# Performance work log

Measured on AMD Instinct MI355X. Metric: run time of the kernel, lower is better.

Reference implementation:

```python
import jax, jax.numpy as jnp
import numpy as np

B, S, H = 2, 2048, 4096
NH, NKV, HD = 32, 8, 128
EPS = 1e-6


def _rope_tables(seq_len, head_dim, base=10000.0):
    inv = 1.0 / (base ** (np.arange(0, head_dim, 2, dtype=np.float32) / head_dim))
    t = np.arange(seq_len, dtype=np.float32)
    freqs = np.outer(t, inv)                       # [S, HD/2]
    emb = np.concatenate([freqs, freqs], axis=-1)  # [S, HD] (HF rotate_half layout)
    return jnp.asarray(np.cos(emb)), jnp.asarray(np.sin(emb))


def setup_inputs() -> dict:
    key = jax.random.key(0)
    ks = jax.random.split(key, 6)
    x = jax.random.normal(ks[0], (B, S, H), dtype=jnp.float32)
    wq = jax.random.normal(ks[1], (NH * HD, H), dtype=jnp.float32) * 0.02
    wk = jax.random.normal(ks[2], (NKV * HD, H), dtype=jnp.float32) * 0.02
    wv = jax.random.normal(ks[3], (NKV * HD, H), dtype=jnp.float32) * 0.02
    wo = jax.random.normal(ks[4], (H, NH * HD), dtype=jnp.float32) * 0.02
    cos1, sin1 = _rope_tables(S, HD)
    cos = jnp.broadcast_to(cos1[None], (B, S, HD))
    sin = jnp.broadcast_to(sin1[None], (B, S, HD))
    return {
        "x": x, "cos": cos, "sin": sin,
        "wq": wq, "wk": wk, "wv": wv, "wo": wo,
        "q_norm_w": jnp.ones((HD,), jnp.float32),
        "k_norm_w": jnp.ones((HD,), jnp.float32),
    }


def _rms_norm(x, w):
    # fp32 RMSNorm over last dim, scaled by per-head-dim weight
    xf = x.astype(jnp.float32)
    n = xf * jax.lax.rsqrt(jnp.mean(xf * xf, axis=-1, keepdims=True) + EPS)
    return n.astype(x.dtype) * w


def _rotate_half(x):
    x1, x2 = jnp.split(x, 2, axis=-1)
    return jnp.concatenate([-x2, x1], axis=-1)


def reference(x, cos, sin, wq, wk, wv, wo, q_norm_w, k_norm_w):
    bs, seqlen, _ = x.shape
    # projections (nn.Linear: y = x @ W^T)
    xq = (x @ wq.T).reshape(bs, seqlen, NH, HD)
    xk = (x @ wk.T).reshape(bs, seqlen, NKV, HD)
    xv = (x @ wv.T).reshape(bs, seqlen, NKV, HD)
    # per-head RMSNorm before RoPE
    xq = _rms_norm(xq, q_norm_w)
    xk = _rms_norm(xk, k_norm_w)
    # [b, h, s, d]
    xq = xq.transpose(0, 2, 1, 3)
    xk = xk.transpose(0, 2, 1, 3)
    xv = xv.transpose(0, 2, 1, 3)
    # RoPE, cos/sin broadcast over heads
    c = cos[:, None, :, :]
    s = sin[:, None, :, :]
    xq = xq * c + _rotate_half(xq) * s
    xk = xk * c + _rotate_half(xk) * s
    # GQA: repeat kv heads
    rep = NH // NKV
    if rep > 1:
        xk = jnp.repeat(xk, rep, axis=1)
        xv = jnp.repeat(xv, rep, axis=1)
    # causal SDPA
    scale = 1.0 / jnp.sqrt(jnp.float32(HD))
    scores = jnp.einsum("bhqd,bhkd->bhqk", xq, xk) * scale
    mask = jnp.tril(jnp.ones((seqlen, seqlen), bool))
    scores = jnp.where(mask, scores, jnp.finfo(scores.dtype).min)
    probs = jax.nn.softmax(scores, axis=-1)
    out = jnp.einsum("bhqk,bhkd->bhqd", probs, xv)
    out = out.transpose(0, 2, 1, 3).reshape(bs, seqlen, NH * HD)
    return out @ wo.T
```

## Files before the change

kernel.cpp:

```cpp
#include <hip/hip_runtime.h>
#include <hip/hip_bf16.h>

#define NB  2
#define SS  2048
#define HH  4096
#define NH  32
#define NKV 8
#define HD  128
#define MR  (NB*SS)

typedef __bf16 bf16x8 __attribute__((ext_vector_type(8)));
typedef float  f32x4  __attribute__((ext_vector_type(4)));
typedef float  f32x16 __attribute__((ext_vector_type(16)));
using bf16 = __hip_bfloat16;

__device__ __forceinline__ f32x4 mfma16(bf16x8 a, bf16x8 b, f32x4 c) {
  return __builtin_amdgcn_mfma_f32_16x16x32_bf16(a, b, c, 0, 0, 0);
}
__device__ __forceinline__ f32x16 mfma32(bf16x8 a, bf16x8 b, f32x16 c) {
  return __builtin_amdgcn_mfma_f32_32x32x16_bf16(a, b, c, 0, 0, 0);
}
__device__ __forceinline__ unsigned cvtpk(float lo, float hi) {
  unsigned r; asm("v_cvt_pk_bf16_f32 %0, %1, %2" : "=v"(r) : "v"(lo), "v"(hi));
  return r;
}
__device__ __forceinline__ void swap32(unsigned &a, unsigned &b) {
  asm volatile("v_permlane32_swap_b32 %0, %1" : "+v"(a), "+v"(b));
}
__device__ __forceinline__ float fexp2(float x) {
  float r; asm("v_exp_f32 %0, %1" : "=v"(r) : "v"(x)); return r;
}

typedef const __attribute__((address_space(1))) void gv_t;
typedef __attribute__((address_space(3))) void lv_t;
__device__ __forceinline__ void gload16(const void* g, void* l) {
  __builtin_amdgcn_global_load_lds((gv_t*)g, (lv_t*)l, 16, 0, 0);
}
#define CFENCE asm volatile("" ::: "memory")

__global__ void f2b5(const float* __restrict__ s0, const float* __restrict__ s1,
                     const float* __restrict__ s2, const float* __restrict__ s3,
                     const float* __restrict__ s4,
                     bf16* __restrict__ d0, bf16* __restrict__ d1,
                     bf16* __restrict__ d2, bf16* __restrict__ d3,
                     bf16* __restrict__ d4)
{
  const unsigned c0 = 4194304u, c1 = 8388608u, c2 = 9437184u, c3 = 10485760u,
                 c4 = 14680064u;
  unsigned i = blockIdx.x*blockDim.x + threadIdx.x;
  unsigned stride = gridDim.x*blockDim.x;
  for (unsigned u = i; u < c4; u += stride) {
    const float* s; bf16* d; unsigned off;
    if (u < c0)      { s = s0; d = d0; off = u; }
    else if (u < c1) { s = s1; d = d1; off = u - c0; }
    else if (u < c2) { s = s2; d = d2; off = u - c1; }
    else if (u < c3) { s = s3; d = d3; off = u - c2; }
    else             { s = s4; d = d4; off = u - c3; }
    float4 v = *(const float4*)(s + (size_t)off*4);
    __hip_bfloat16 b0 = __float2bfloat16(v.x);
    __hip_bfloat16 b1 = __float2bfloat16(v.y);
    __hip_bfloat16 b2 = __float2bfloat16(v.z);
    __hip_bfloat16 b3 = __float2bfloat16(v.w);
    ushort4 o;
    o.x = *reinterpret_cast<unsigned short*>(&b0);
    o.y = *reinterpret_cast<unsigned short*>(&b1);
    o.z = *reinterpret_cast<unsigned short*>(&b2);
    o.w = *reinterpret_cast<unsigned short*>(&b3);
    *(ushort4*)((unsigned short*)d + (size_t)off*4) = o;
  }
}

template<typename OutT>
__global__ __launch_bounds__(512, 2) void gemm256(
    const bf16* __restrict__ A, const bf16* __restrict__ Bt, OutT* __restrict__ C,
    int M, int N, int K, int tilesX)
{
  __shared__ bf16 lds[2*2*2*8192];

  const int bid = blockIdx.x;
  const int cpx = gridDim.x >> 3;
  const int wg  = (bid & 7)*cpx + (bid >> 3);
  const int m0 = (wg / tilesX) * 256, n0 = (wg % tilesX) * 256;

  const int tid = threadIdx.x;
  const int l = tid & 63;
  const int l15 = l & 15, lhi = l >> 4;
  const int wid = tid >> 6;
  const int wr = wid >> 2, wc = wid & 3;

  const int srow = tid >> 2;
  const int sps  = tid & 3;
  const int sls  = (sps - (srow >> 1)) & 3;
  const bf16* ga0 = A  + (size_t)(m0 + srow)*K       + sls*8;
  const bf16* ga1 = A  + (size_t)(m0 + srow + 128)*K + sls*8;
  const bf16* gb0 = Bt + (size_t)(n0 + srow)*K       + sls*8;
  const bf16* gb1 = Bt + (size_t)(n0 + srow + 128)*K + sls*8;
  const int ldst = tid*8;

#define REG(buf, mat, ks) (&lds[(((buf)*2 + (mat))*2 + (ks))*8192])
#define STG_A(buf, ks, kofs) do {                                 \
    gload16(ga0 + (kofs), REG(buf,0,ks) + ldst);                  \
    gload16(ga1 + (kofs), REG(buf,0,ks) + ldst + 4096);           \
  } while (0)
#define STG_B(buf, ks, kofs) do {                                 \
    gload16(gb0 + (kofs), REG(buf,1,ks) + ldst);                  \
    gload16(gb1 + (kofs), REG(buf,1,ks) + ldst + 4096);           \
  } while (0)

  f32x4 acc[8][4];
  #pragma unroll
  for (int fm = 0; fm < 8; ++fm)
    #pragma unroll
    for (int fn = 0; fn < 4; ++fn)
      #pragma unroll
      for (int e = 0; e < 4; ++e) acc[fm][fn][e] = 0.f;

  const int arow = wr*128 + l15;
  const int brow = wc*64  + l15;
  const int psl  = (lhi + (l15 >> 1)) & 3;

#define PHASE(PB, KS, STG, WN) do {                                        \
    const bf16* Ar_ = REG(PB, 0, KS);                                      \
    const bf16* Br_ = REG(PB, 1, KS);                                      \
    bf16x8 af[8], bv[4];                                                   \
    for (int fm = 0; fm < 8; ++fm)                                         \
      af[fm] = *(const bf16x8*)(Ar_ + (arow + fm*16)*32 + psl*8);          \
    for (int fn = 0; fn < 4; ++fn)                                         \
      bv[fn] = *(const bf16x8*)(Br_ + (brow + fn*16)*32 + psl*8);          \
    STG;                                                                   \
    CFENCE;                                                                \
    __builtin_amdgcn_s_barrier();                                          \
    __builtin_amdgcn_s_setprio(1);                                         \
    for (int fm = 0; fm < 8; ++fm)                                         \
      for (int fn = 0; fn < 4; ++fn)                                       \
        acc[fm][fn] = mfma16(af[fm], bv[fn], acc[fm][fn]);                 \
    __builtin_amdgcn_s_setprio(0);                                         \
    if ((WN) == 8)      asm volatile("s_waitcnt vmcnt(8)" ::: "memory");   \
    else if ((WN) == 4) asm volatile("s_waitcnt vmcnt(4)" ::: "memory");   \
    else if ((WN) == 0) asm volatile("s_waitcnt vmcnt(0)" ::: "memory");   \
    __builtin_amdgcn_s_barrier();                                          \
    CFENCE;                                                                \
  } while (0)

  const int nt = K >> 6;

  STG_A(0, 0, 0);  STG_B(0, 0, 0);
  STG_A(0, 1, 32); STG_B(0, 1, 32);
  STG_A(1, 0, 64); STG_B(1, 0, 64);
  asm volatile("s_waitcnt vmcnt(8)" ::: "memory");
  __builtin_amdgcn_s_barrier();
  CFENCE;

  for (int i = 0; i < (nt >> 1) - 1; ++i) {
    const int t  = i << 1;
    const int k1 = ((t + 1) << 6) + 32;
    const int k2 = (t + 2) << 6;
    const int k3 = (t + 3) << 6;
    PHASE(0, 0, { STG_A(1, 1, k1);      STG_B(1, 1, k1);      }, 8);
    PHASE(0, 1, { STG_A(0, 0, k2);      STG_B(0, 0, k2);      }, 8);
    PHASE(1, 0, { STG_A(0, 1, k2 + 32); STG_B(0, 1, k2 + 32); }, 8);
    PHASE(1, 1, { STG_A(1, 0, k3);      STG_B(1, 0, k3);      }, 8);
  }
  {
    const int k1 = ((nt - 1) << 6) + 32;
    PHASE(0, 0, { STG_A(1, 1, k1); STG_B(1, 1, k1); }, 8);
    PHASE(0, 1, (void)0,  4);
    PHASE(1, 0, (void)0,  0);
    PHASE(1, 1, (void)0, -1);
  }
#undef PHASE
#undef STG_A
#undef STG_B
#undef REG

  #pragma unroll
  for (int fm = 0; fm < 8; ++fm) {
    const int crow = m0 + wr*128 + fm*16 + lhi*4;
    #pragma unroll
    for (int fn = 0; fn < 4; ++fn) {
      const int ccol = n0 + wc*64 + fn*16 + l15;
      #pragma unroll
      for (int j = 0; j < 4; ++j) {
        if constexpr (sizeof(OutT) == 2)
          C[(size_t)(crow + j)*N + ccol] = __float2bfloat16(acc[fm][fn][j]);
        else
          C[(size_t)(crow + j)*N + ccol] = acc[fm][fn][j];
      }
    }
  }
}

__global__ __launch_bounds__(512, 2) void gemm128n(
    const bf16* __restrict__ A, const bf16* __restrict__ Bt, bf16* __restrict__ C,
    int M, int N, int K, int tilesX)
{
  __shared__ bf16 lds[2*2*12288];

  const int bid = blockIdx.x;
  const int cpx = gridDim.x >> 3;
  const int wg  = (bid & 7)*cpx + (bid >> 3);
  const int m0 = (wg / tilesX) * 128, n0 = (wg % tilesX) * 256;

  const int tid = threadIdx.x;
  const int l = tid & 63;
  const int l15 = l & 15, lhi = l >> 4;
  const int wid = tid >> 6;
  const int wr = wid >> 2, wc = wid & 3;

  const int srow = tid >> 2;
  const int sps  = tid & 3;
  const int sls  = (sps - (srow >> 1)) & 3;
  const bf16* gaA = A  + (size_t)(m0 + srow)*K       + sls*8;
  const bf16* gb0 = Bt + (size_t)(n0 + srow)*K       + sls*8;
  const bf16* gb1 = Bt + (size_t)(n0 + srow + 128)*K + sls*8;
  const int ldst = tid*8;

#define REGA(buf, ks) (&lds[((buf)*2 + (ks))*12288])
#define REGB(buf, ks) (&lds[((buf)*2 + (ks))*12288 + 4096])
#define STGKA(buf, ks, kofs) gload16(gaA + (kofs), REGA(buf,ks) + ldst)
#define STGKB(buf, ks, kofs) do {                                 \
    gload16(gb0 + (kofs), REGB(buf,ks) + ldst);                   \
    gload16(gb1 + (kofs), REGB(buf,ks) + ldst + 4096);            \
  } while (0)

  f32x4 acc[4][4];
  #pragma unroll
  for (int fm = 0; fm < 4; ++fm)
    #pragma unroll
    for (int fn = 0; fn < 4; ++fn)
      #pragma unroll
      for (int e = 0; e < 4; ++e) acc[fm][fn][e] = 0.f;

  const int arow = wr*64 + l15;
  const int brow = wc*64 + l15;
  const int psl  = (lhi + (l15 >> 1)) & 3;

#define PHASEK(PB, KS, STG, WN) do {                                       \
    const bf16* Ar_ = REGA(PB, KS);                                        \
    const bf16* Br_ = REGB(PB, KS);                                        \
    bf16x8 af[4], bv[4];                                                   \
    for (int fm = 0; fm < 4; ++fm)                                         \
      af[fm] = *(const bf16x8*)(Ar_ + (arow + fm*16)*32 + psl*8);          \
    for (int fn = 0; fn < 4; ++fn)                                         \
      bv[fn] = *(const bf16x8*)(Br_ + (brow + fn*16)*32 + psl*8);          \
    STG;                                                                   \
    CFENCE;                                                                \
    __builtin_amdgcn_s_barrier();                                          \
    __builtin_amdgcn_s_setprio(1);                                         \
    for (int fm = 0; fm < 4; ++fm)                                         \
      for (int fn = 0; fn < 4; ++fn)                                       \
        acc[fm][fn] = mfma16(af[fm], bv[fn], acc[fm][fn]);                 \
    __builtin_amdgcn_s_setprio(0);                                         \
    if ((WN) == 6)      asm volatile("s_waitcnt vmcnt(6)" ::: "memory");   \
    else if ((WN) == 0) asm volatile("s_waitcnt vmcnt(0)" ::: "memory");   \
    __builtin_amdgcn_s_barrier();                                          \
    CFENCE;                                                                \
  } while (0)

  const int nt = K >> 6;

  STGKB(0, 0, 0);  STGKA(0, 0, 0);  STGKB(0, 1, 32);  STGKA(0, 1, 32);
  STGKB(1, 0, 64); STGKA(1, 0, 64); STGKB(1, 1, 96);  STGKA(1, 1, 96);
  asm volatile("s_waitcnt vmcnt(6)" ::: "memory");
  __builtin_amdgcn_s_barrier();
  CFENCE;

  for (int i = 0; i < (nt >> 1) - 1; ++i) {
    const int t  = i << 1;
    const int k2 = (t + 2) << 6;
    const int k3 = (t + 3) << 6;
    PHASEK(0, 0, { STGKB(0, 0, k2);      STGKA(0, 0, k2);      }, -1);
    PHASEK(0, 1, { STGKB(0, 1, k2 + 32); STGKA(0, 1, k2 + 32); },  6);
    PHASEK(1, 0, { STGKB(1, 0, k3);      STGKA(1, 0, k3);      }, -1);
    PHASEK(1, 1, { STGKB(1, 1, k3 + 32); STGKA(1, 1, k3 + 32); },  6);
  }
  {
    PHASEK(0, 0, (void)0, -1);
    PHASEK(0, 1, (void)0,  0);
    PHASEK(1, 0, (void)0, -1);
    PHASEK(1, 1, (void)0, -1);
  }
#undef PHASEK
#undef STGKA
#undef STGKB
#undef REGA
#undef REGB

  #pragma unroll
  for (int fm = 0; fm < 4; ++fm) {
    const int crow = m0 + wr*64 + fm*16 + lhi*4;
    #pragma unroll
    for (int fn = 0; fn < 4; ++fn) {
      const int ccol = n0 + wc*64 + fn*16 + l15;
      #pragma unroll
      for (int j = 0; j < 4; ++j)
        C[(size_t)(crow + j)*N + ccol] = __float2bfloat16(acc[fm][fn][j]);
    }
  }
}

__global__ __launch_bounds__(256) void normrope(
    const bf16* __restrict__ src, bf16* __restrict__ dst,
    const float* __restrict__ cosb, const float* __restrict__ sinb,
    const float* __restrict__ w, int nh, float scale, int rowstride, int coloff)
{
  const int wid = threadIdx.x >> 6, lane = threadIdx.x & 63;
  const int row = blockIdx.x*4 + wid;
  const int m = row / nh, h = row % nh;
  const int b = m / SS, s = m % SS;
  const bf16* sp = src + (size_t)m*rowstride + coloff + h*HD;
  float v1 = __bfloat162float(sp[lane]);
  float v2 = __bfloat162float(sp[lane + 64]);
  float ss = v1*v1 + v2*v2;
  #pragma unroll
  for (int msk = 1; msk < 64; msk <<= 1) ss += __shfl_xor(ss, msk);
  float r = rsqrtf(ss*(1.f/128.f) + 1e-6f) * scale;
  float n1 = v1*r*w[lane], n2 = v2*r*w[lane + 64];
  const float* cp  = cosb + (size_t)m*HD;
  const float* sip = sinb + (size_t)m*HD;
  float o1 = n1*cp[lane]      - n2*sip[lane];
  float o2 = n2*cp[lane + 64] + n1*sip[lane + 64];
  bf16* dp = dst + ((size_t)(b*nh + h)*SS + s)*HD;
  dp[lane]      = __float2bfloat16(o1);
  dp[lane + 64] = __float2bfloat16(o2);
}

__global__ __launch_bounds__(256) void vtrans(const bf16* __restrict__ v0,
                                              bf16* __restrict__ vt,
                                              int rowstride, int coloff)
{
  __shared__ bf16 tile[64][65];
  const int s0 = blockIdx.x*64, d0 = blockIdx.y*64, bkv = blockIdx.z;
  const int bb = bkv >> 3, kv = bkv & 7;
  const int c = threadIdx.x & 63, rbase = threadIdx.x >> 6;
  #pragma unroll
  for (int r = 0; r < 64; r += 4) {
    int sl = r + rbase;
    tile[sl][c] = v0[(size_t)(bb*SS + s0 + sl)*rowstride + coloff + kv*HD + d0 + c];
  }
  __syncthreads();
  #pragma unroll
  for (int r = 0; r < 64; r += 4) {
    int dl = r + rbase;
    vt[((size_t)bkv*HD + d0 + dl)*SS + s0 + c] = tile[c][dl];
  }
}

__global__ __launch_bounds__(512, 2) void attn_fwd(
    const bf16* __restrict__ qr, const bf16* __restrict__ kr,
    const bf16* __restrict__ vt, bf16* __restrict__ ao)
{
  __shared__ __align__(16) char smem[65536];

  const int L = blockIdx.x;
  const int orig = (L & 7)*64 + (L >> 3);
  const int bh = orig >> 3, j = orig & 7;
  const int b = bh >> 5, h = bh & 31, kvh = h >> 2;

  const int tid = threadIdx.x;
  const int wid = tid >> 6, lane = tid & 63;
  const int l31 = lane & 31, hi = lane >> 5;
  const unsigned hi16 = hi << 4;
  const unsigned swz = (lane & 7) << 4;

  const int qw0 = (wid < 4) ? (j*128 + wid*32) : ((15 - j)*128 + (wid - 4)*32);
  const int NT = 32 - 2*j;
  const int qlane = qw0 + l31;

  const bf16* Qp = qr + ((size_t)(b*NH + h)*SS + qlane)*HD;
  const bf16* Kp = kr + (size_t)(b*NKV + kvh)*SS*HD;
  const bf16* Vp = vt + (size_t)(b*NKV + kvh)*HD*SS;

  const int krA = tid >> 4;
  const int ksA = tid & 15;
  const int vrA = tid >> 3;
  const int vsA = tid & 7;
  const int kswz = (ksA ^ (krA & 7))*8;
  const int vswz = (vsA ^ (vrA & 7))*8;

#define STAGE_ATTN(buf, kvbase) do {                                        \
    char* kb = smem + (buf)*32768;                                          \
    char* vb = kb + 16384;                                                  \
    gload16(Kp + (size_t)(krA + (kvbase))*HD + kswz,      kb + tid*16);     \
    gload16(Kp + (size_t)(krA + 32 + (kvbase))*HD + kswz, kb + 8192 + tid*16); \
    gload16(Vp + (size_t)vrA*SS + (kvbase) + vswz,        vb + tid*16);     \
    gload16(Vp + (size_t)(vrA + 64)*SS + (kvbase) + vswz, vb + 8192 + tid*16); \
  } while (0)

  STAGE_ATTN(0, 0);
  bf16x8 qf[8];
  #pragma unroll
  for (int kd = 0; kd < 8; ++kd)
    qf[kd] = *(const bf16x8*)(Qp + kd*16 + hi*8);
  asm volatile("s_waitcnt vmcnt(0)" ::: "memory");
  __builtin_amdgcn_s_barrier();
  CFENCE;

  f32x16 o0, o1, o2, o3;
  #pragma unroll
  for (int r = 0; r < 16; ++r) { o0[r] = 0.f; o1[r] = 0.f; o2[r] = 0.f; o3[r] = 0.f; }
  float mrow = -1e30f, lrow = 0.f;

  for (int t = 0; t < NT; ++t) {
    const int p = t & 1;
    const char* KsB = smem + p*32768;
    const char* VsB = KsB + 16384;
    if (t + 1 < NT) STAGE_ATTN(p ^ 1, (t + 1)*64);
    const int kv0 = t*64;

    if (kv0 <= qw0 + 31) {
      f32x16 s0, s1;
      #pragma unroll
      for (int r = 0; r < 16; ++r) { s0[r] = 0.f; s1[r] = 0.f; }
      __builtin_amdgcn_s_setprio(1);
      #pragma unroll
      for (int kd = 0; kd < 8; ++kd) {
        bf16x8 k0f = *(const bf16x8*)(KsB + l31*256        + (((unsigned)(kd*32) + hi16) ^ swz));
        bf16x8 k1f = *(const bf16x8*)(KsB + (32 + l31)*256 + (((unsigned)(kd*32) + hi16) ^ swz));
        s0 = mfma32(k0f, qf[kd], s0);
        s1 = mfma32(k1f, qf[kd], s1);
      }
      __builtin_amdgcn_s_setprio(0);
      if (kv0 + 63 > qw0) {
        #pragma unroll
        for (int r = 0; r < 16; ++r) {
          const int off = (r & 3) + 8*(r >> 2) + 4*hi;
          if (kv0 + off > qlane)      s0[r] = -1e30f;
          if (kv0 + 32 + off > qlane) s1[r] = -1e30f;
        }
      }
      float mg[8];
      #pragma unroll
      for (int r = 0; r < 8; ++r)
        mg[r] = fmaxf(fmaxf(s0[r], s0[r + 8]), fmaxf(s1[r], s1[r + 8]));
      float ta = fmaxf(fmaxf(mg[0], mg[1]), mg[2]);
      float tb = fmaxf(fmaxf(mg[3], mg[4]), mg[5]);
      float tmax = fmaxf(fmaxf(ta, tb), fmaxf(mg[6], mg[7]));
      tmax = fmaxf(tmax, __shfl_xor(tmax, 32));
      if (!__all(tmax <= mrow + 8.f)) {
        float mnew = fmaxf(mrow, tmax);
        float alpha = fexp2(mrow - mnew);
        mrow = mnew;
        lrow *= alpha;
        #pragma unroll
        for (int r = 0; r < 16; ++r) {
          o0[r] *= alpha; o1[r] *= alpha; o2[r] *= alpha; o3[r] *= alpha;
        }
      }
      float tsum = 0.f;
      #pragma unroll
      for (int r = 0; r < 16; ++r) { s0[r] = fexp2(s0[r] - mrow); tsum += s0[r]; }
      #pragma unroll
      for (int r = 0; r < 16; ++r) { s1[r] = fexp2(s1[r] - mrow); tsum += s1[r]; }
      tsum += __shfl_xor(tsum, 32);
      lrow += tsum;

      #pragma unroll
      for (int ks = 0; ks < 4; ++ks) {
        const int bb0 = (ks & 1)*8;
        float p0,p1,p2,p3,p4,p5,p6,p7;
        if (ks < 2) { p0=s0[bb0+0];p1=s0[bb0+1];p2=s0[bb0+2];p3=s0[bb0+3];
                      p4=s0[bb0+4];p5=s0[bb0+5];p6=s0[bb0+6];p7=s0[bb0+7]; }
        else        { p0=s1[bb0+0];p1=s1[bb0+1];p2=s1[bb0+2];p3=s1[bb0+3];
                      p4=s1[bb0+4];p5=s1[bb0+5];p6=s1[bb0+6];p7=s1[bb0+7]; }
        unsigned c01 = cvtpk(p0,p1), c23 = cvtpk(p2,p3);
        unsigned c45 = cvtpk(p4,p5), c67 = cvtpk(p6,p7);
        unsigned w0 = c01, w2 = c45; swap32(w0, w2);
        unsigned w1 = c23, w3 = c67; swap32(w1, w3);
        union { unsigned u[4]; bf16x8 v; } pa;
        pa.u[0]=w0; pa.u[1]=w1; pa.u[2]=w2; pa.u[3]=w3;
        __builtin_amdgcn_s_setprio(1);
        #pragma unroll
        for (int dt = 0; dt < 4; ++dt) {
          bf16x8 vf = *(const bf16x8*)(VsB + (dt*32 + l31)*128 +
                                       (((unsigned)(ks*32) + hi16) ^ swz));
          f32x16 &oo = (dt==0)?o0:(dt==1)?o1:(dt==2)?o2:o3;
          oo = mfma32(vf, pa.v, oo);
        }
        __builtin_amdgcn_s_setprio(0);
      }
    }

    asm volatile("s_waitcnt vmcnt(0)" ::: "memory");
    __builtin_amdgcn_s_barrier();
    CFENCE;
  }
#undef STAGE_ATTN

  const float invl = 1.f / lrow;
  char* ow = smem + wid*4096;
  bf16* aop = ao + ((size_t)b*SS + qlane)*HH + h*HD;
  const unsigned eswz = (l31 & 7) << 4;
  #pragma unroll
  for (int half = 0; half < 2; ++half) {
    #pragma unroll
    for (int hh = 0; hh < 2; ++hh) {
      #pragma unroll
      for (int r = 0; r < 16; ++r) {
        const int dcol = hh*32 + (r & 3) + 8*(r >> 2) + 4*hi;
        float val = ((half*2+hh)==0 ? o0[r] : (half*2+hh)==1 ? o1[r]
                     : (half*2+hh)==2 ? o2[r] : o3[r]) * invl;
        *(bf16*)(ow + l31*128 + (((unsigned)(dcol*2)) ^ eswz)) = __float2bfloat16(val);
      }
    }
    #pragma unroll
    for (int m = 0; m < 4; ++m) {
      const int c0 = hi*32 + m*8;
      bf16x8 vv = *(const bf16x8*)(ow + l31*128 + (((unsigned)(c0*2)) ^ eswz));
      *(bf16x8*)(aop + half*64 + c0) = vv;
    }
  }
}

extern "C" void kernel_launch(void* const* d_in, const int* in_sizes, int n_in,
                              void* d_out, int out_size, void* d_ws, size_t ws_size,
                              hipStream_t stream)
{
  const float* x    = (const float*)d_in[0];
  const float* cosb = (const float*)d_in[1];
  const float* sinb = (const float*)d_in[2];
  const float* wq   = (const float*)d_in[3];
  const float* wk   = (const float*)d_in[4];
  const float* wv   = (const float*)d_in[5];
  const float* wo   = (const float*)d_in[6];
  const float* qnw  = (const float*)d_in[7];
  const float* knw  = (const float*)d_in[8];
  float* out = (float*)d_out;

  char* ws = (char*)d_ws;
  bf16* xb    = (bf16*)(ws);
  bf16* wqkvb = (bf16*)(ws +  33554432);
  bf16* wob   = (bf16*)(ws +  83886080);
  bf16* q0    = (bf16*)(ws + 117440512);
  bf16* kv0   = (bf16*)(ws + 150994944);
  bf16* qr    = (bf16*)(ws + 167772160);
  bf16* vt = xb;
  bf16* kr = (bf16*)(ws + 8388608);
  bf16* ao = q0;

  f2b5<<<2048, 256, 0, stream>>>(x, wq, wk, wv, wo,
                                 xb, wqkvb,
                                 wqkvb + (size_t)4096*4096,
                                 wqkvb + (size_t)5120*4096,
                                 wob);

  gemm256<bf16><<<256, 512, 0, stream>>>(xb, wqkvb, q0, MR, 4096, HH, 16);
  gemm128n<<<256, 512, 0, stream>>>(xb, wqkvb + (size_t)4096*4096, kv0,
                                    MR, 2048, HH, 8);

  normrope<<<(MR*NH)/4,  256, 0, stream>>>(q0, qr, cosb, sinb, qnw, NH,
                                           0.08838834764831845f*1.44269504088896341f,
                                           4096, 0);
  normrope<<<(MR*NKV)/4, 256, 0, stream>>>(kv0, kr, cosb, sinb, knw, NKV, 1.0f,
                                           2048, 0);
  vtrans<<<dim3(32, 2, 16), 256, 0, stream>>>(kv0, vt, 2048, 1024);

  attn_fwd<<<512, 512, 0, stream>>>(qr, kr, vt, ao);

  gemm256<float><<<256, 512, 0, stream>>>(ao, wob, out, MR, HH, HH, 16);
}
```

Before: 535.9 us.

## Use 16-wave GEMM tiles and drop attention XCD swizzle and setprio

The 256x256 GEMM now launches 1024 threads (16 waves), so each wave computes a 64x64 sub-tile instead of 128x64. Each thread stages one A row and one B row, and the vmcnt wait counts are halved to match. The attention kernel drops its XCD-aware block remapping in favour of a linear (j, bh) mapping and removes the s_setprio hints around its MFMA loops. These changes trade lower per-wave register pressure for less per-wave data reuse, more LDS reads per MFMA and an aggressive launch-bound occupancy hint that may constrain register allocation.

```diff
diff --git a/kernel.cpp b/kernel.cpp
--- a/kernel.cpp
+++ b/kernel.cpp
@@ -71,7 +71,7 @@
 }
 
 template<typename OutT>
-__global__ __launch_bounds__(512, 2) void gemm256(
+__global__ __launch_bounds__(1024, 4) void gemm256(
     const bf16* __restrict__ A, const bf16* __restrict__ Bt, OutT* __restrict__ C,
     int M, int N, int K, int tilesX)
 {
@@ -91,39 +91,33 @@
   const int srow = tid >> 2;
   const int sps  = tid & 3;
   const int sls  = (sps - (srow >> 1)) & 3;
-  const bf16* ga0 = A  + (size_t)(m0 + srow)*K       + sls*8;
-  const bf16* ga1 = A  + (size_t)(m0 + srow + 128)*K + sls*8;
-  const bf16* gb0 = Bt + (size_t)(n0 + srow)*K       + sls*8;
-  const bf16* gb1 = Bt + (size_t)(n0 + srow + 128)*K + sls*8;
+  const bf16* ga = A  + (size_t)(m0 + srow)*K + sls*8;
+  const bf16* gb = Bt + (size_t)(n0 + srow)*K + sls*8;
   const int ldst = tid*8;
 
 #define REG(buf, mat, ks) (&lds[(((buf)*2 + (mat))*2 + (ks))*8192])
-#define STG_A(buf, ks, kofs) do {                                 \
-    gload16(ga0 + (kofs), REG(buf,0,ks) + ldst);                  \
-    gload16(ga1 + (kofs), REG(buf,0,ks) + ldst + 4096);           \
+#define STG_AB(buf, ks, kofs) do {                                \
+    gload16(ga + (kofs), REG(buf,0,ks) + ldst);                   \
+    gload16(gb + (kofs), REG(buf,1,ks) + ldst);                   \
   } while (0)
-#define STG_B(buf, ks, kofs) do {                                 \
-    gload16(gb0 + (kofs), REG(buf,1,ks) + ldst);                  \
-    gload16(gb1 + (kofs), REG(buf,1,ks) + ldst + 4096);           \
-  } while (0)
-
-  f32x4 acc[8][4];
-  #pragma unroll
-  for (int fm = 0; fm < 8; ++fm)
+
+  f32x4 acc[4][4];
+  #pragma unroll
+  for (int fm = 0; fm < 4; ++fm)
     #pragma unroll
     for (int fn = 0; fn < 4; ++fn)
       #pragma unroll
       for (int e = 0; e < 4; ++e) acc[fm][fn][e] = 0.f;
 
-  const int arow = wr*128 + l15;
-  const int brow = wc*64  + l15;
+  const int arow = wr*64 + l15;
+  const int brow = wc*64 + l15;
   const int psl  = (lhi + (l15 >> 1)) & 3;
 
 #define PHASE(PB, KS, STG, WN) do {                                        \
     const bf16* Ar_ = REG(PB, 0, KS);                                      \
     const bf16* Br_ = REG(PB, 1, KS);                                      \
-    bf16x8 af[8], bv[4];                                                   \
-    for (int fm = 0; fm < 8; ++fm)                                         \
+    bf16x8 af[4], bv[4];                                                   \
+    for (int fm = 0; fm < 4; ++fm)                                         \
       af[fm] = *(const bf16x8*)(Ar_ + (arow + fm*16)*32 + psl*8);          \
     for (int fn = 0; fn < 4; ++fn)                                         \
       bv[fn] = *(const bf16x8*)(Br_ + (brow + fn*16)*32 + psl*8);          \
@@ -131,12 +125,12 @@
     CFENCE;                                                                \
     __builtin_amdgcn_s_barrier();                                          \
     __builtin_amdgcn_s_setprio(1);                                         \
-    for (int fm = 0; fm < 8; ++fm)                                         \
+    for (int fm = 0; fm < 4; ++fm)                                         \
       for (int fn = 0; fn < 4; ++fn)                                       \
         acc[fm][fn] = mfma16(af[fm], bv[fn], acc[fm][fn]);                 \
     __builtin_amdgcn_s_setprio(0);                                         \
-    if ((WN) == 8)      asm volatile("s_waitcnt vmcnt(8)" ::: "memory");   \
-    else if ((WN) == 4) asm volatile("s_waitcnt vmcnt(4)" ::: "memory");   \
+    if ((WN) == 4)      asm volatile("s_waitcnt vmcnt(4)" ::: "memory");   \
+    else if ((WN) == 2) asm volatile("s_waitcnt vmcnt(2)" ::: "memory");   \
     else if ((WN) == 0) asm volatile("s_waitcnt vmcnt(0)" ::: "memory");   \
     __builtin_amdgcn_s_barrier();                                          \
     CFENCE;                                                                \
@@ -144,10 +138,8 @@
 
   const int nt = K >> 6;
 
-  STG_A(0, 0, 0);  STG_B(0, 0, 0);
-  STG_A(0, 1, 32); STG_B(0, 1, 32);
-  STG_A(1, 0, 64); STG_B(1, 0, 64);
-  asm volatile("s_waitcnt vmcnt(8)" ::: "memory");
+  STG_AB(0, 0, 0); STG_AB(0, 1, 32); STG_AB(1, 0, 64);
+  asm volatile("s_waitcnt vmcnt(4)" ::: "memory");
   __builtin_amdgcn_s_barrier();
   CFENCE;
 
@@ -156,26 +148,25 @@
     const int k1 = ((t + 1) << 6) + 32;
     const int k2 = (t + 2) << 6;
     const int k3 = (t + 3) << 6;
-    PHASE(0, 0, { STG_A(1, 1, k1);      STG_B(1, 1, k1);      }, 8);
-    PHASE(0, 1, { STG_A(0, 0, k2);      STG_B(0, 0, k2);      }, 8);
-    PHASE(1, 0, { STG_A(0, 1, k2 + 32); STG_B(0, 1, k2 + 32); }, 8);
-    PHASE(1, 1, { STG_A(1, 0, k3);      STG_B(1, 0, k3);      }, 8);
+    PHASE(0, 0, STG_AB(1, 1, k1),      4);
+    PHASE(0, 1, STG_AB(0, 0, k2),      4);
+    PHASE(1, 0, STG_AB(0, 1, k2 + 32), 4);
+    PHASE(1, 1, STG_AB(1, 0, k3),      4);
   }
   {
     const int k1 = ((nt - 1) << 6) + 32;
-    PHASE(0, 0, { STG_A(1, 1, k1); STG_B(1, 1, k1); }, 8);
-    PHASE(0, 1, (void)0,  4);
-    PHASE(1, 0, (void)0,  0);
-    PHASE(1, 1, (void)0, -1);
+    PHASE(0, 0, STG_AB(1, 1, k1), 4);
+    PHASE(0, 1, (void)0,          2);
+    PHASE(1, 0, (void)0,          0);
+    PHASE(1, 1, (void)0,         -1);
   }
 #undef PHASE
-#undef STG_A
-#undef STG_B
+#undef STG_AB
 #undef REG
 
   #pragma unroll
-  for (int fm = 0; fm < 8; ++fm) {
-    const int crow = m0 + wr*128 + fm*16 + lhi*4;
+  for (int fm = 0; fm < 4; ++fm) {
+    const int crow = m0 + wr*64 + fm*16 + lhi*4;
     #pragma unroll
     for (int fn = 0; fn < 4; ++fn) {
       const int ccol = n0 + wc*64 + fn*16 + l15;
@@ -353,8 +344,8 @@
   __shared__ __align__(16) char smem[65536];
 
   const int L = blockIdx.x;
-  const int orig = (L & 7)*64 + (L >> 3);
-  const int bh = orig >> 3, j = orig & 7;
+  const int j = L >> 6;
+  const int bh = L & 63;
   const int b = bh >> 5, h = bh & 31, kvh = h >> 2;
 
   const int tid = threadIdx.x;
@@ -412,7 +403,6 @@
       f32x16 s0, s1;
       #pragma unroll
       for (int r = 0; r < 16; ++r) { s0[r] = 0.f; s1[r] = 0.f; }
-      __builtin_amdgcn_s_setprio(1);
       #pragma unroll
       for (int kd = 0; kd < 8; ++kd) {
         bf16x8 k0f = *(const bf16x8*)(KsB + l31*256        + (((unsigned)(kd*32) + hi16) ^ swz));
@@ -420,7 +410,6 @@
         s0 = mfma32(k0f, qf[kd], s0);
         s1 = mfma32(k1f, qf[kd], s1);
       }
-      __builtin_amdgcn_s_setprio(0);
       if (kv0 + 63 > qw0) {
         #pragma unroll
         for (int r = 0; r < 16; ++r) {
@@ -469,7 +458,6 @@
         unsigned w1 = c23, w3 = c67; swap32(w1, w3);
         union { unsigned u[4]; bf16x8 v; } pa;
         pa.u[0]=w0; pa.u[1]=w1; pa.u[2]=w2; pa.u[3]=w3;
-        __builtin_amdgcn_s_setprio(1);
         #pragma unroll
         for (int dt = 0; dt < 4; ++dt) {
           bf16x8 vf = *(const bf16x8*)(VsB + (dt*32 + l31)*128 +
@@ -477,7 +465,6 @@
           f32x16 &oo = (dt==0)?o0:(dt==1)?o1:(dt==2)?o2:o3;
           oo = mfma32(vf, pa.v, oo);
         }
-        __builtin_amdgcn_s_setprio(0);
       }
     }
 
@@ -544,7 +531,7 @@
                                  wqkvb + (size_t)5120*4096,
                                  wob);
 
-  gemm256<bf16><<<256, 512, 0, stream>>>(xb, wqkvb, q0, MR, 4096, HH, 16);
+  gemm256<bf16><<<256, 1024, 0, stream>>>(xb, wqkvb, q0, MR, 4096, HH, 16);
   gemm128n<<<256, 512, 0, stream>>>(xb, wqkvb + (size_t)4096*4096, kv0,
                                     MR, 2048, HH, 8);
 
@@ -557,5 +544,5 @@
 
   attn_fwd<<<512, 512, 0, stream>>>(qr, kr, vt, ao);
 
-  gemm256<float><<<256, 512, 0, stream>>>(ao, wob, out, MR, HH, HH, 16);
-}
+  gemm256<float><<<256, 1024, 0, stream>>>(ao, wob, out, MR, HH, HH, 16);
+}
```

New measurement: 522.7 us. 2.5% less time.
